# Kernel tuning notes

Hardware: AMD Instinct MI355X
Metric: run time of the kernel (lower is better)

## Reference

```python
import jax, jax.numpy as jnp
import numpy as np

W = 0.5  # loss weight from __init__
EPS = 1e-14


def gradient_l2_loss(x):
    """Mean squared forward finite-difference along each spatial axis of (B,s,r,c)."""
    loss = 0.0
    for ax in (1, 2, 3):
        d = jnp.diff(x, axis=ax)
        loss = loss + jnp.mean(d * d)
    return loss


def setup_inputs() -> dict:
    key = jax.random.key(0)
    k1, k2 = jax.random.split(key)
    B, S, R, C = 2, 128, 128, 128
    L = jax.random.normal(k1, (B, 3, S, R, C), dtype=jnp.float32)
    U = jax.random.normal(k2, (B, 9, S, R, C), dtype=jnp.float32)
    return {"L": L, "U": U}


def reference(L, U):
    B, _, S, R, C = U.shape
    # torch.sort(L, dim=1, descending=True) -> indices[:,0] == argmax over the 3 eigenvalues
    idx0 = jnp.argmax(L, axis=1)  # (B,S,R,C) int
    # U channel layout U{row}_{col}: reshape to (B, col=3, row=3, S,R,C)
    Uview = U.reshape(B, 3, 3, S, R, C)
    idx = jnp.broadcast_to(idx0[:, None, None], (B, 3, 1, S, R, C))
    # faithful to original gather(dim=2)[:, :, 0]
    major = jnp.take_along_axis(Uview, idx, axis=2)[:, :, 0]  # (B,3,S,R,C)
    am = jnp.abs(major)
    den = jnp.sum(am * am, axis=1)  # (B,S,R,C)
    den = jnp.where(den < EPS, EPS, den)
    e1, e2, e3 = am[:, 0], am[:, 1], am[:, 2]
    CO = jnp.sqrt(0.5 * ((e1 - e2) ** 2 + (e2 - e3) ** 2 + (e3 - e1) ** 2) / den)
    CO_grad = 0.0
    for i in range(9):  # fixed small channel loop
        CO_grad = CO_grad + gradient_l2_loss(U[:, i])
    return (CO + CO_grad).mean() * W
```

## Files before the change

kernel.cpp:

```cpp
#include <hip/hip_runtime.h>

#define SS 128
#define RR 128
#define CC 128
#define EPSF 1e-14f

__global__ __launch_bounds__(256) void scol_main(const float* __restrict__ L,
                                                 const float* __restrict__ U,
                                                 float4* __restrict__ part,
                                                 int nvec) {
    const int SRC = SS * RR * CC;
    const int CV = CC / 4;

    float a_co = 0.f, a_ds = 0.f, a_dr = 0.f, a_dc = 0.f;

    int t = blockIdx.x * blockDim.x + threadIdx.x;
    if (t < nvec) {
        int c4 = t % CV;
        int r  = (t / CV) % RR;
        int s  = (t / (CV * RR)) % SS;
        int b  = t / (CV * RR * SS);
        int c  = c4 * 4;

        int pos    = ((s * RR) + r) * CC + c;
        int base_l = b * 3 * SRC + pos;
        int base_u = b * 9 * SRC + pos;

        float4 l0 = *(const float4*)(L + base_l);
        float4 l1 = *(const float4*)(L + base_l + SRC);
        float4 l2 = *(const float4*)(L + base_l + 2 * SRC);
        float L0[4] = {l0.x, l0.y, l0.z, l0.w};
        float L1[4] = {l1.x, l1.y, l1.z, l1.w};
        float L2[4] = {l2.x, l2.y, l2.z, l2.w};
        int idx[4];
#pragma unroll
        for (int j = 0; j < 4; ++j) {
            int id = 0;
            float best = L0[j];
            if (L1[j] > best) { best = L1[j]; id = 1; }
            if (L2[j] > best) { best = L2[j]; id = 2; }
            idx[j] = id;
        }

        float am[3][4];
#pragma unroll
        for (int g = 0; g < 3; ++g)
#pragma unroll
            for (int j = 0; j < 4; ++j) am[g][j] = 0.f;

        bool has_c = (c4 < CV - 1);
        bool has_r = (r < RR - 1);
        bool has_s = (s < SS - 1);

#pragma unroll
        for (int ch = 0; ch < 9; ++ch) {
            int o = base_u + ch * SRC;
            float4 u = *(const float4*)(U + o);
            float uu[4] = {u.x, u.y, u.z, u.w};

            int g = ch / 3, m = ch % 3;
#pragma unroll
            for (int j = 0; j < 4; ++j)
                if (idx[j] == m) am[g][j] = fabsf(uu[j]);

            float d;
            d = u.y - u.x; a_dc += d * d;
            d = u.z - u.y; a_dc += d * d;
            d = u.w - u.z; a_dc += d * d;
            if (has_c) { float un = U[o + 4]; d = un - u.w; a_dc += d * d; }
            if (has_r) {
                float4 ur = *(const float4*)(U + o + CC);
                d = ur.x - u.x; a_dr += d * d;
                d = ur.y - u.y; a_dr += d * d;
                d = ur.z - u.z; a_dr += d * d;
                d = ur.w - u.w; a_dr += d * d;
            }
            if (has_s) {
                float4 us = *(const float4*)(U + o + RR * CC);
                d = us.x - u.x; a_ds += d * d;
                d = us.y - u.y; a_ds += d * d;
                d = us.z - u.z; a_ds += d * d;
                d = us.w - u.w; a_ds += d * d;
            }
        }

#pragma unroll
        for (int j = 0; j < 4; ++j) {
            float e1 = am[0][j], e2 = am[1][j], e3 = am[2][j];
            float den = e1 * e1 + e2 * e2 + e3 * e3;
            den = fmaxf(den, EPSF);
            float num = 0.5f * ((e1 - e2) * (e1 - e2) + (e2 - e3) * (e2 - e3) +
                                (e3 - e1) * (e3 - e1));
            a_co += sqrtf(num / den);
        }
    }

#pragma unroll
    for (int off = 32; off > 0; off >>= 1) {
        a_co += __shfl_down(a_co, off);
        a_ds += __shfl_down(a_ds, off);
        a_dr += __shfl_down(a_dr, off);
        a_dc += __shfl_down(a_dc, off);
    }

    __shared__ float s_co[4], s_ds[4], s_dr[4], s_dc[4];
    int wid = threadIdx.x >> 6;
    int lane = threadIdx.x & 63;
    if (lane == 0) {
        s_co[wid] = a_co; s_ds[wid] = a_ds;
        s_dr[wid] = a_dr; s_dc[wid] = a_dc;
    }
    __syncthreads();
    if (threadIdx.x == 0) {
        float t_co = 0.f, t_ds = 0.f, t_dr = 0.f, t_dc = 0.f;
        for (int w = 0; w < 4; ++w) {
            t_co += s_co[w]; t_ds += s_ds[w];
            t_dr += s_dr[w]; t_dc += s_dc[w];
        }
        part[blockIdx.x] = make_float4(t_co, t_ds, t_dr, t_dc);
    }
}

__global__ __launch_bounds__(256) void scol_final(const float4* __restrict__ part,
                                                  float* __restrict__ out,
                                                  int nblk, int B) {
    double d_co = 0., d_ds = 0., d_dr = 0., d_dc = 0.;
    for (int i = threadIdx.x; i < nblk; i += blockDim.x) {
        float4 p = part[i];
        d_co += (double)p.x; d_ds += (double)p.y;
        d_dr += (double)p.z; d_dc += (double)p.w;
    }
#pragma unroll
    for (int off = 32; off > 0; off >>= 1) {
        d_co += __shfl_down(d_co, off);
        d_ds += __shfl_down(d_ds, off);
        d_dr += __shfl_down(d_dr, off);
        d_dc += __shfl_down(d_dc, off);
    }
    __shared__ double sh[4][4];
    int wid = threadIdx.x >> 6;
    int lane = threadIdx.x & 63;
    if (lane == 0) {
        sh[wid][0] = d_co; sh[wid][1] = d_ds;
        sh[wid][2] = d_dr; sh[wid][3] = d_dc;
    }
    __syncthreads();
    if (threadIdx.x == 0) {
        double t_co = 0., t_ds = 0., t_dr = 0., t_dc = 0.;
        for (int w = 0; w < 4; ++w) {
            t_co += sh[w][0]; t_ds += sh[w][1];
            t_dr += sh[w][2]; t_dc += sh[w][3];
        }
        double nvox = (double)B * SS * RR * CC;
        double nds  = (double)B * (SS - 1) * RR * CC;
        double ndr  = (double)B * SS * (RR - 1) * CC;
        double ndc  = (double)B * SS * RR * (CC - 1);
        out[0] = (float)(0.5 * (t_co / nvox + t_ds / nds + t_dr / ndr + t_dc / ndc));
    }
}

extern "C" void kernel_launch(void* const* d_in, const int* in_sizes, int n_in,
                              void* d_out, int out_size, void* d_ws, size_t ws_size,
                              hipStream_t stream) {
    const float* L = (const float*)d_in[0];
    const float* U = (const float*)d_in[1];
    float* out = (float*)d_out;

    int B = in_sizes[1] / (9 * SS * RR * CC);
    int nvec = B * SS * RR * (CC / 4);

    int threads = 256;
    int blocks = (nvec + threads - 1) / threads;

    float4* part = (float4*)d_ws;

    hipLaunchKernelGGL(scol_main, dim3(blocks), dim3(threads), 0, stream,
                       L, U, part, nvec);
    hipLaunchKernelGGL(scol_final, dim3(1), dim3(threads), 0, stream,
                       part, out, blocks, B);
}
```

Measured before the change: 252.8 us.

## Hoist all U loads up front, use lane shuffle for column neighbor, branchless edges

Restructures the main kernel so each thread issues all 9 center, row-neighbor and slice-neighbor float4 loads before any arithmetic, raising memory-level parallelism. The scalar column-neighbor load is replaced by a wavefront shuffle from the adjacent lane. Edge conditions become clamped offsets and 0/1 weights, so there are no branches. This costs more registers (27 float4 held live), which the launch bounds of 2 are meant to cap.

Result: faster. 245.4 us (-3.0%).

```diff
diff --git a/kernel.cpp b/kernel.cpp
--- a/kernel.cpp
+++ b/kernel.cpp
@@ -5,94 +5,110 @@
 #define CC 128
 #define EPSF 1e-14f
 
-__global__ __launch_bounds__(256) void scol_main(const float* __restrict__ L,
-                                                 const float* __restrict__ U,
-                                                 float4* __restrict__ part,
-                                                 int nvec) {
+__global__ __launch_bounds__(256, 2) void scol_main(const float* __restrict__ L,
+                                                    const float* __restrict__ U,
+                                                    float4* __restrict__ part) {
     const int SRC = SS * RR * CC;
-    const int CV = CC / 4;
 
-    float a_co = 0.f, a_ds = 0.f, a_dr = 0.f, a_dc = 0.f;
+    int tid = threadIdx.x;
+    int c4  = tid & 31;
+    int row = blockIdx.x * 8 + (tid >> 5);
+    int r   = row & (RR - 1);
+    int sr  = row >> 7;
+    int s   = sr & (SS - 1);
+    int b   = sr >> 7;
+    int c   = c4 << 2;
 
-    int t = blockIdx.x * blockDim.x + threadIdx.x;
-    if (t < nvec) {
-        int c4 = t % CV;
-        int r  = (t / CV) % RR;
-        int s  = (t / (CV * RR)) % SS;
-        int b  = t / (CV * RR * SS);
-        int c  = c4 * 4;
+    int pos    = (row - b * (SS * RR)) * CC + c;
+    int base_l = b * 3 * SRC + pos;
+    int base_u = b * 9 * SRC + pos;
 
-        int pos    = ((s * RR) + r) * CC + c;
-        int base_l = b * 3 * SRC + pos;
-        int base_u = b * 9 * SRC + pos;
+    bool  hr = (r < RR - 1), hs = (s < SS - 1), hc = (c4 < 31);
+    float wr = hr ? 1.f : 0.f;
+    float ws = hs ? 1.f : 0.f;
+    float wc = hc ? 1.f : 0.f;
+    int offr = hr ? CC : 0;
+    int offs = hs ? RR * CC : 0;
 
-        float4 l0 = *(const float4*)(L + base_l);
-        float4 l1 = *(const float4*)(L + base_l + SRC);
-        float4 l2 = *(const float4*)(L + base_l + 2 * SRC);
-        float L0[4] = {l0.x, l0.y, l0.z, l0.w};
-        float L1[4] = {l1.x, l1.y, l1.z, l1.w};
-        float L2[4] = {l2.x, l2.y, l2.z, l2.w};
-        int idx[4];
+    float4 l0 = *(const float4*)(L + base_l);
+    float4 l1 = *(const float4*)(L + base_l + SRC);
+    float4 l2 = *(const float4*)(L + base_l + 2 * SRC);
+
+    float4 u[9], ur[9], us[9];
 #pragma unroll
-        for (int j = 0; j < 4; ++j) {
-            int id = 0;
-            float best = L0[j];
-            if (L1[j] > best) { best = L1[j]; id = 1; }
-            if (L2[j] > best) { best = L2[j]; id = 2; }
-            idx[j] = id;
-        }
+    for (int ch = 0; ch < 9; ++ch) {
+        const float* p = U + base_u + ch * SRC;
+        u[ch] = *(const float4*)(p);
+    }
+#pragma unroll
+    for (int ch = 0; ch < 9; ++ch) {
+        const float* p = U + base_u + ch * SRC;
+        ur[ch] = *(const float4*)(p + offr);
+        us[ch] = *(const float4*)(p + offs);
+    }
 
-        float am[3][4];
+    float L0[4] = {l0.x, l0.y, l0.z, l0.w};
+    float L1[4] = {l1.x, l1.y, l1.z, l1.w};
+    float L2[4] = {l2.x, l2.y, l2.z, l2.w};
+    int idx[4];
 #pragma unroll
-        for (int g = 0; g < 3; ++g)
+    for (int j = 0; j < 4; ++j) {
+        int id = 0;
+        float best = L0[j];
+        if (L1[j] > best) { best = L1[j]; id = 1; }
+        if (L2[j] > best) { best = L2[j]; id = 2; }
+        idx[j] = id;
+    }
+
+    float am[3][4];
 #pragma unroll
-            for (int j = 0; j < 4; ++j) am[g][j] = 0.f;
+    for (int g = 0; g < 3; ++g)
+#pragma unroll
+        for (int j = 0; j < 4; ++j) am[g][j] = 0.f;
 
-        bool has_c = (c4 < CV - 1);
-        bool has_r = (r < RR - 1);
-        bool has_s = (s < SS - 1);
+    float a_dc = 0.f, t_dcb = 0.f, t_dr = 0.f, t_ds = 0.f;
 
 #pragma unroll
-        for (int ch = 0; ch < 9; ++ch) {
-            int o = base_u + ch * SRC;
-            float4 u = *(const float4*)(U + o);
-            float uu[4] = {u.x, u.y, u.z, u.w};
+    for (int ch = 0; ch < 9; ++ch) {
+        float4 uu = u[ch];
+        float uuv[4] = {uu.x, uu.y, uu.z, uu.w};
+        int g = ch / 3, m = ch % 3;
+#pragma unroll
+        for (int j = 0; j < 4; ++j)
+            if (idx[j] == m) am[g][j] = fabsf(uuv[j]);
 
-            int g = ch / 3, m = ch % 3;
+        float d;
+        d = uu.y - uu.x; a_dc += d * d;
+        d = uu.z - uu.y; a_dc += d * d;
+        d = uu.w - uu.z; a_dc += d * d;
+        float un = __shfl_down(uu.x, 1);
+        d = un - uu.w; t_dcb += d * d;
+
+        float4 R4 = ur[ch];
+        d = R4.x - uu.x; t_dr += d * d;
+        d = R4.y - uu.y; t_dr += d * d;
+        d = R4.z - uu.z; t_dr += d * d;
+        d = R4.w - uu.w; t_dr += d * d;
+
+        float4 S4 = us[ch];
+        d = S4.x - uu.x; t_ds += d * d;
+        d = S4.y - uu.y; t_ds += d * d;
+        d = S4.z - uu.z; t_ds += d * d;
+        d = S4.w - uu.w; t_ds += d * d;
+    }
+    a_dc += wc * t_dcb;
+    float a_dr = wr * t_dr;
+    float a_ds = ws * t_ds;
+
+    float a_co = 0.f;
 #pragma unroll
-            for (int j = 0; j < 4; ++j)
-                if (idx[j] == m) am[g][j] = fabsf(uu[j]);
-
-            float d;
-            d = u.y - u.x; a_dc += d * d;
-            d = u.z - u.y; a_dc += d * d;
-            d = u.w - u.z; a_dc += d * d;
-            if (has_c) { float un = U[o + 4]; d = un - u.w; a_dc += d * d; }
-            if (has_r) {
-                float4 ur = *(const float4*)(U + o + CC);
-                d = ur.x - u.x; a_dr += d * d;
-                d = ur.y - u.y; a_dr += d * d;
-                d = ur.z - u.z; a_dr += d * d;
-                d = ur.w - u.w; a_dr += d * d;
-            }
-            if (has_s) {
-                float4 us = *(const float4*)(U + o + RR * CC);
-                d = us.x - u.x; a_ds += d * d;
-                d = us.y - u.y; a_ds += d * d;
-                d = us.z - u.z; a_ds += d * d;
-                d = us.w - u.w; a_ds += d * d;
-            }
-        }
-
-#pragma unroll
-        for (int j = 0; j < 4; ++j) {
-            float e1 = am[0][j], e2 = am[1][j], e3 = am[2][j];
-            float den = e1 * e1 + e2 * e2 + e3 * e3;
-            den = fmaxf(den, EPSF);
-            float num = 0.5f * ((e1 - e2) * (e1 - e2) + (e2 - e3) * (e2 - e3) +
-                                (e3 - e1) * (e3 - e1));
-            a_co += sqrtf(num / den);
-        }
+    for (int j = 0; j < 4; ++j) {
+        float e1 = am[0][j], e2 = am[1][j], e3 = am[2][j];
+        float den = e1 * e1 + e2 * e2 + e3 * e3;
+        den = fmaxf(den, EPSF);
+        float num = 0.5f * ((e1 - e2) * (e1 - e2) + (e2 - e3) * (e2 - e3) +
+                            (e3 - e1) * (e3 - e1));
+        a_co += sqrtf(num / den);
     }
 
 #pragma unroll
@@ -104,7 +120,7 @@
     }
 
     __shared__ float s_co[4], s_ds[4], s_dr[4], s_dc[4];
-    int wid = threadIdx.x >> 6;
+    int wid  = threadIdx.x >> 6;
     int lane = threadIdx.x & 63;
     if (lane == 0) {
         s_co[wid] = a_co; s_ds[wid] = a_ds;
@@ -112,12 +128,12 @@
     }
     __syncthreads();
     if (threadIdx.x == 0) {
-        float t_co = 0.f, t_ds = 0.f, t_dr = 0.f, t_dc = 0.f;
+        float t_co = 0.f, t_s = 0.f, t_r = 0.f, t_c = 0.f;
         for (int w = 0; w < 4; ++w) {
-            t_co += s_co[w]; t_ds += s_ds[w];
-            t_dr += s_dr[w]; t_dc += s_dc[w];
+            t_co += s_co[w]; t_s += s_ds[w];
+            t_r += s_dr[w]; t_c += s_dc[w];
         }
-        part[blockIdx.x] = make_float4(t_co, t_ds, t_dr, t_dc);
+        part[blockIdx.x] = make_float4(t_co, t_s, t_r, t_c);
     }
 }
 
@@ -138,7 +154,7 @@
         d_dc += __shfl_down(d_dc, off);
     }
     __shared__ double sh[4][4];
-    int wid = threadIdx.x >> 6;
+    int wid  = threadIdx.x >> 6;
     int lane = threadIdx.x & 63;
     if (lane == 0) {
         sh[wid][0] = d_co; sh[wid][1] = d_ds;
@@ -167,15 +183,13 @@
     float* out = (float*)d_out;
 
     int B = in_sizes[1] / (9 * SS * RR * CC);
-    int nvec = B * SS * RR * (CC / 4);
-
-    int threads = 256;
-    int blocks = (nvec + threads - 1) / threads;
+    int nrow = B * SS * RR;
+    int blocks = nrow / 8;
 
     float4* part = (float4*)d_ws;
 
-    hipLaunchKernelGGL(scol_main, dim3(blocks), dim3(threads), 0, stream,
-                       L, U, part, nvec);
-    hipLaunchKernelGGL(scol_final, dim3(1), dim3(threads), 0, stream,
+    hipLaunchKernelGGL(scol_main, dim3(blocks), dim3(256), 0, stream,
+                       L, U, part);
+    hipLaunchKernelGGL(scol_final, dim3(1), dim3(256), 0, stream,
                        part, out, blocks, B);
 }
```

## Stream s-slabs through double-buffered LDS with async global-to-LDS loads

Applied to the files above, without the earlier changes.

Replaces the one-thread-per-voxel-vector kernel with blocks that each own a 4-row by 8-slice tile. The tile is streamed along s with double-buffered LDS filled by global_load_lds DMA, and the previous slice is kept in registers for the s-difference. This removes the redundant neighbour reads in r and s, which roughly tripled U traffic, and overlaps the next slice's load with compute. The cost is fewer blocks (1024 of 128 threads), which lowers parallelism, plus per-slice barriers. It also depends on exact LDS layout indexing for the boundary row.

Result: slower. 261.8 us (+3.6%).

```diff
diff --git a/kernel.cpp b/kernel.cpp
--- a/kernel.cpp
+++ b/kernel.cpp
@@ -1,92 +1,149 @@
 #include <hip/hip_runtime.h>
+#include <stdint.h>
 
 #define SS 128
 #define RR 128
 #define CC 128
+#define RC (RR * CC)
+#define SRC (SS * RC)
+#define LS 8
 #define EPSF 1e-14f
 
-__global__ __launch_bounds__(256) void scol_main(const float* __restrict__ L,
-                                                 const float* __restrict__ U,
-                                                 float4* __restrict__ part,
-                                                 int nvec) {
-    const int SRC = SS * RR * CC;
-    const int CV = CC / 4;
+#define SLAB_F 4608
+#define BND_F 1152
+#define BUF_F (SLAB_F + BND_F)
+
+__device__ __forceinline__ void dma16(const float* g, float* l) {
+    __builtin_amdgcn_global_load_lds(
+        (const __attribute__((address_space(1))) uint32_t*)g,
+        (__attribute__((address_space(3))) uint32_t*)l,
+        16, 0, 0);
+}
+
+__global__ __launch_bounds__(128, 4) void scol_main(const float* __restrict__ L,
+                                                    const float* __restrict__ U,
+                                                    float4* __restrict__ part) {
+    __shared__ float lds[2][BUF_F];
+    __shared__ float sred[2][4];
+
+    const int tid = threadIdx.x;
+    const int c4  = tid & 31;
+    const int row = tid >> 5;
+
+    int g   = blockIdx.x;
+    int rcI = g & 31;
+    int scI = (g >> 5) & 15;
+    int b   = g >> 9;
+
+    int r0 = rcI << 2;
+    int s0 = scI << 3;
+    int r  = r0 + row;
+    int c  = c4 << 2;
+
+    const float* Ub = U + (size_t)b * 9 * SRC;
+    const float* Lb = L + (size_t)b * 3 * SRC;
+
+    float wc = (c4 < 31) ? 1.f : 0.f;
+    float wr = (r < RR - 1) ? 1.f : 0.f;
+    int rowb = (r0 + 4 < RR) ? (r0 + 4) : (RR - 1);
+
+    float4 uprev[9];
+    {
+        int sprev = (s0 > 0) ? (s0 - 1) : 0;
+        const float* p = Ub + sprev * RC + r * CC + c;
+#pragma unroll
+        for (int ch = 0; ch < 9; ++ch)
+            uprev[ch] = *(const float4*)(p + ch * SRC);
+    }
+
+    {
+        float* dst = &lds[0][0];
+        const float* srcP = Ub + s0 * RC + r0 * CC;
+#pragma unroll
+        for (int ch = 0; ch < 9; ++ch)
+            dma16(srcP + ch * SRC + tid * 4, dst + ch * 512 + tid * 4);
+        const float* srcB = Ub + s0 * RC + rowb * CC;
+        int chp = tid >> 5, col = c4 << 2;
+        dma16(srcB + chp * SRC + col,       dst + SLAB_F + tid * 4);
+        dma16(srcB + (chp + 4) * SRC + col, dst + SLAB_F + 512 + tid * 4);
+        if (tid < 32)
+            dma16(srcB + 8 * SRC + col,     dst + SLAB_F + 1024 + tid * 4);
+    }
 
     float a_co = 0.f, a_ds = 0.f, a_dr = 0.f, a_dc = 0.f;
 
-    int t = blockIdx.x * blockDim.x + threadIdx.x;
-    if (t < nvec) {
-        int c4 = t % CV;
-        int r  = (t / CV) % RR;
-        int s  = (t / (CV * RR)) % SS;
-        int b  = t / (CV * RR * SS);
-        int c  = c4 * 4;
-
-        int pos    = ((s * RR) + r) * CC + c;
-        int base_l = b * 3 * SRC + pos;
-        int base_u = b * 9 * SRC + pos;
-
-        float4 l0 = *(const float4*)(L + base_l);
-        float4 l1 = *(const float4*)(L + base_l + SRC);
-        float4 l2 = *(const float4*)(L + base_l + 2 * SRC);
-        float L0[4] = {l0.x, l0.y, l0.z, l0.w};
-        float L1[4] = {l1.x, l1.y, l1.z, l1.w};
-        float L2[4] = {l2.x, l2.y, l2.z, l2.w};
-        int idx[4];
+    for (int i = 0; i < LS; ++i) {
+        int s  = s0 + i;
+        int bb = i & 1;
+
+        __syncthreads();
+
+        if (i < LS - 1) {
+            float* dst = &lds[bb ^ 1][0];
+            int sp = s + 1;
+            const float* srcP = Ub + sp * RC + r0 * CC;
+#pragma unroll
+            for (int ch = 0; ch < 9; ++ch)
+                dma16(srcP + ch * SRC + tid * 4, dst + ch * 512 + tid * 4);
+            const float* srcB = Ub + sp * RC + rowb * CC;
+            int chp = tid >> 5, col = c4 << 2;
+            dma16(srcB + chp * SRC + col,       dst + SLAB_F + tid * 4);
+            dma16(srcB + (chp + 4) * SRC + col, dst + SLAB_F + 512 + tid * 4);
+            if (tid < 32)
+                dma16(srcB + 8 * SRC + col,     dst + SLAB_F + 1024 + tid * 4);
+        }
+
+        const float* lp = Lb + s * RC + r * CC + c;
+        float4 l0 = *(const float4*)(lp);
+        float4 l1 = *(const float4*)(lp + SRC);
+        float4 l2 = *(const float4*)(lp + 2 * SRC);
+
+        const float* buf  = &lds[bb][0];
+        const float* ownB = buf + row * 128 + c;
+        const float* rnB  = (row < 3) ? (buf + (row + 1) * 128 + c)
+                                      : (buf + SLAB_F + c);
+        int rnStride = (row < 3) ? 512 : 128;
+
+        float wsd = (s > 0) ? 1.f : 0.f;
+
+        float t_ds = 0.f, t_dr = 0.f, t_dcb = 0.f;
+#pragma unroll
+        for (int ch = 0; ch < 9; ++ch) {
+            float4 own = *(const float4*)(ownB + ch * 512);
+            float4 rn  = *(const float4*)(rnB + ch * rnStride);
+            float  cn  = *(ownB + ch * 512 + 4);
+            float d;
+            d = own.y - own.x; a_dc += d * d;
+            d = own.z - own.y; a_dc += d * d;
+            d = own.w - own.z; a_dc += d * d;
+            d = cn    - own.w; t_dcb += d * d;
+            d = rn.x - own.x; t_dr += d * d;
+            d = rn.y - own.y; t_dr += d * d;
+            d = rn.z - own.z; t_dr += d * d;
+            d = rn.w - own.w; t_dr += d * d;
+            float4 up = uprev[ch];
+            d = own.x - up.x; t_ds += d * d;
+            d = own.y - up.y; t_ds += d * d;
+            d = own.z - up.z; t_ds += d * d;
+            d = own.w - up.w; t_ds += d * d;
+            uprev[ch] = own;
+        }
+        a_dc += wc * t_dcb;
+        a_dr += wr * t_dr;
+        a_ds += wsd * t_ds;
+
+        float Lv0[4] = {l0.x, l0.y, l0.z, l0.w};
+        float Lv1[4] = {l1.x, l1.y, l1.z, l1.w};
+        float Lv2[4] = {l2.x, l2.y, l2.z, l2.w};
 #pragma unroll
         for (int j = 0; j < 4; ++j) {
             int id = 0;
-            float best = L0[j];
-            if (L1[j] > best) { best = L1[j]; id = 1; }
-            if (L2[j] > best) { best = L2[j]; id = 2; }
-            idx[j] = id;
-        }
-
-        float am[3][4];
-#pragma unroll
-        for (int g = 0; g < 3; ++g)
-#pragma unroll
-            for (int j = 0; j < 4; ++j) am[g][j] = 0.f;
-
-        bool has_c = (c4 < CV - 1);
-        bool has_r = (r < RR - 1);
-        bool has_s = (s < SS - 1);
-
-#pragma unroll
-        for (int ch = 0; ch < 9; ++ch) {
-            int o = base_u + ch * SRC;
-            float4 u = *(const float4*)(U + o);
-            float uu[4] = {u.x, u.y, u.z, u.w};
-
-            int g = ch / 3, m = ch % 3;
-#pragma unroll
-            for (int j = 0; j < 4; ++j)
-                if (idx[j] == m) am[g][j] = fabsf(uu[j]);
-
-            float d;
-            d = u.y - u.x; a_dc += d * d;
-            d = u.z - u.y; a_dc += d * d;
-            d = u.w - u.z; a_dc += d * d;
-            if (has_c) { float un = U[o + 4]; d = un - u.w; a_dc += d * d; }
-            if (has_r) {
-                float4 ur = *(const float4*)(U + o + CC);
-                d = ur.x - u.x; a_dr += d * d;
-                d = ur.y - u.y; a_dr += d * d;
-                d = ur.z - u.z; a_dr += d * d;
-                d = ur.w - u.w; a_dr += d * d;
-            }
-            if (has_s) {
-                float4 us = *(const float4*)(U + o + RR * CC);
-                d = us.x - u.x; a_ds += d * d;
-                d = us.y - u.y; a_ds += d * d;
-                d = us.z - u.z; a_ds += d * d;
-                d = us.w - u.w; a_ds += d * d;
-            }
-        }
-
-#pragma unroll
-        for (int j = 0; j < 4; ++j) {
-            float e1 = am[0][j], e2 = am[1][j], e3 = am[2][j];
+            float best = Lv0[j];
+            if (Lv1[j] > best) { best = Lv1[j]; id = 1; }
+            if (Lv2[j] > best) { best = Lv2[j]; id = 2; }
+            float e1 = fabsf(*(ownB + (0 + id) * 512 + j));
+            float e2 = fabsf(*(ownB + (3 + id) * 512 + j));
+            float e3 = fabsf(*(ownB + (6 + id) * 512 + j));
             float den = e1 * e1 + e2 * e2 + e3 * e3;
             den = fmaxf(den, EPSF);
             float num = 0.5f * ((e1 - e2) * (e1 - e2) + (e2 - e3) * (e2 - e3) +
@@ -102,22 +159,17 @@
         a_dr += __shfl_down(a_dr, off);
         a_dc += __shfl_down(a_dc, off);
     }
-
-    __shared__ float s_co[4], s_ds[4], s_dr[4], s_dc[4];
-    int wid = threadIdx.x >> 6;
-    int lane = threadIdx.x & 63;
+    int wid = tid >> 6, lane = tid & 63;
     if (lane == 0) {
-        s_co[wid] = a_co; s_ds[wid] = a_ds;
-        s_dr[wid] = a_dr; s_dc[wid] = a_dc;
+        sred[wid][0] = a_co; sred[wid][1] = a_ds;
+        sred[wid][2] = a_dr; sred[wid][3] = a_dc;
     }
     __syncthreads();
-    if (threadIdx.x == 0) {
-        float t_co = 0.f, t_ds = 0.f, t_dr = 0.f, t_dc = 0.f;
-        for (int w = 0; w < 4; ++w) {
-            t_co += s_co[w]; t_ds += s_ds[w];
-            t_dr += s_dr[w]; t_dc += s_dc[w];
-        }
-        part[blockIdx.x] = make_float4(t_co, t_ds, t_dr, t_dc);
+    if (tid == 0) {
+        part[blockIdx.x] = make_float4(sred[0][0] + sred[1][0],
+                                       sred[0][1] + sred[1][1],
+                                       sred[0][2] + sred[1][2],
+                                       sred[0][3] + sred[1][3]);
     }
 }
 
@@ -138,8 +190,7 @@
         d_dc += __shfl_down(d_dc, off);
     }
     __shared__ double sh[4][4];
-    int wid = threadIdx.x >> 6;
-    int lane = threadIdx.x & 63;
+    int wid = threadIdx.x >> 6, lane = threadIdx.x & 63;
     if (lane == 0) {
         sh[wid][0] = d_co; sh[wid][1] = d_ds;
         sh[wid][2] = d_dr; sh[wid][3] = d_dc;
@@ -167,15 +218,12 @@
     float* out = (float*)d_out;
 
     int B = in_sizes[1] / (9 * SS * RR * CC);
-    int nvec = B * SS * RR * (CC / 4);
-
-    int threads = 256;
-    int blocks = (nvec + threads - 1) / threads;
+    int blocks = B * 32 * 16;
 
     float4* part = (float4*)d_ws;
 
-    hipLaunchKernelGGL(scol_main, dim3(blocks), dim3(threads), 0, stream,
-                       L, U, part, nvec);
-    hipLaunchKernelGGL(scol_final, dim3(1), dim3(threads), 0, stream,
+    hipLaunchKernelGGL(scol_main, dim3(blocks), dim3(128), 0, stream,
+                       L, U, part);
+    hipLaunchKernelGGL(scol_final, dim3(1), dim3(256), 0, stream,
                        part, out, blocks, B);
 }
```

## Split work across wavefronts by channel group with LDS exchange for argmax gather

Applied to the files above, without the earlier changes.

Each block now covers two rows of one slice. Three wavefronts each load one group of three U channels and compute its finite differences, while the fourth wavefront loads L and computes the argmax indices. Results are exchanged through shared memory and the CO term is computed by the L wave. The column-edge neighbour now comes from a wave shuffle instead of a scalar reload, branches are replaced by multiplicative masks, block ids are remapped XCD-aware, and the final reduction uses 1024 threads. This aims to raise memory-level parallelism and cut redundant loads, at the cost of two extra block barriers and uneven load across the four waves.

Result: no change. 249.8 us (-1.2%).

```diff
diff --git a/kernel.cpp b/kernel.cpp
--- a/kernel.cpp
+++ b/kernel.cpp
@@ -3,94 +3,136 @@
 #define SS 128
 #define RR 128
 #define CC 128
+#define RC (RR * CC)
+#define VOL (SS * RC)
 #define EPSF 1e-14f
 
-__global__ __launch_bounds__(256) void scol_main(const float* __restrict__ L,
-                                                 const float* __restrict__ U,
-                                                 float4* __restrict__ part,
-                                                 int nvec) {
-    const int SRC = SS * RR * CC;
-    const int CV = CC / 4;
+__global__ __launch_bounds__(256, 8) void scol_main(const float* __restrict__ L,
+                                                    const float* __restrict__ U,
+                                                    float4* __restrict__ part,
+                                                    int nblocks) {
+    __shared__ int    lidx[64];
+    __shared__ float4 lde[3][64];
+    __shared__ float  sred[4][4];
+
+    const int tid  = threadIdx.x;
+    const int wid  = tid >> 6;
+    const int lane = tid & 63;
+    const int half = lane >> 5;
+    const int c4   = lane & 31;
+
+    int id = blockIdx.x;
+    if ((nblocks & 7) == 0) {
+        int per = nblocks >> 3;
+        id = (blockIdx.x & 7) * per + (blockIdx.x >> 3);
+    }
+
+    int rp = id & 63;
+    int s  = (id >> 6) & (SS - 1);
+    int b  = id / (64 * SS);
+
+    int r = rp * 2 + half;
+    int c = c4 << 2;
+
+    float wc = (c4 < 31) ? 1.f : 0.f;
+    float wr = (r < RR - 1) ? 1.f : 0.f;
+    float ws = (s < SS - 1) ? 1.f : 0.f;
+    int offr = (r < RR - 1) ? CC : 0;
+    int offs = (s < SS - 1) ? RC : 0;
+
+    size_t posPlane = (size_t)s * RC + (size_t)r * CC + c;
 
     float a_co = 0.f, a_ds = 0.f, a_dr = 0.f, a_dc = 0.f;
 
-    int t = blockIdx.x * blockDim.x + threadIdx.x;
-    if (t < nvec) {
-        int c4 = t % CV;
-        int r  = (t / CV) % RR;
-        int s  = (t / (CV * RR)) % SS;
-        int b  = t / (CV * RR * SS);
-        int c  = c4 * 4;
-
-        int pos    = ((s * RR) + r) * CC + c;
-        int base_l = b * 3 * SRC + pos;
-        int base_u = b * 9 * SRC + pos;
-
-        float4 l0 = *(const float4*)(L + base_l);
-        float4 l1 = *(const float4*)(L + base_l + SRC);
-        float4 l2 = *(const float4*)(L + base_l + 2 * SRC);
-        float L0[4] = {l0.x, l0.y, l0.z, l0.w};
-        float L1[4] = {l1.x, l1.y, l1.z, l1.w};
-        float L2[4] = {l2.x, l2.y, l2.z, l2.w};
-        int idx[4];
+    float4 own[3];
+
+    if (wid < 3) {
+        const float* p0 = U + ((size_t)(b * 9 + 3 * wid)) * VOL + posPlane;
+        float4 sn[3], rn[3];
+#pragma unroll
+        for (int k = 0; k < 3; ++k) {
+            const float* p = p0 + (size_t)k * VOL;
+            own[k] = *(const float4*)(p);
+            sn[k]  = *(const float4*)(p + offs);
+            rn[k]  = *(const float4*)(p + offr);
+        }
+        float t_dcb = 0.f, t_dr = 0.f, t_ds = 0.f;
+#pragma unroll
+        for (int k = 0; k < 3; ++k) {
+            float4 o = own[k];
+            float d;
+            d = o.y - o.x; a_dc += d * d;
+            d = o.z - o.y; a_dc += d * d;
+            d = o.w - o.z; a_dc += d * d;
+            float cn = __shfl_down(o.x, 1);
+            d = cn - o.w; t_dcb += d * d;
+            float4 R4 = rn[k];
+            d = R4.x - o.x; t_dr += d * d;
+            d = R4.y - o.y; t_dr += d * d;
+            d = R4.z - o.z; t_dr += d * d;
+            d = R4.w - o.w; t_dr += d * d;
+            float4 S4 = sn[k];
+            d = S4.x - o.x; t_ds += d * d;
+            d = S4.y - o.y; t_ds += d * d;
+            d = S4.z - o.z; t_ds += d * d;
+            d = S4.w - o.w; t_ds += d * d;
+        }
+        a_dc += wc * t_dcb;
+        a_dr  = wr * t_dr;
+        a_ds  = ws * t_ds;
+    } else {
+        const float* lp = L + ((size_t)(b * 3)) * VOL + posPlane;
+        float4 l0 = *(const float4*)(lp);
+        float4 l1 = *(const float4*)(lp + VOL);
+        float4 l2 = *(const float4*)(lp + 2 * VOL);
+        float A0[4] = {l0.x, l0.y, l0.z, l0.w};
+        float A1[4] = {l1.x, l1.y, l1.z, l1.w};
+        float A2[4] = {l2.x, l2.y, l2.z, l2.w};
+        int pk = 0;
 #pragma unroll
         for (int j = 0; j < 4; ++j) {
-            int id = 0;
-            float best = L0[j];
-            if (L1[j] > best) { best = L1[j]; id = 1; }
-            if (L2[j] > best) { best = L2[j]; id = 2; }
-            idx[j] = id;
-        }
-
-        float am[3][4];
-#pragma unroll
-        for (int g = 0; g < 3; ++g)
-#pragma unroll
-            for (int j = 0; j < 4; ++j) am[g][j] = 0.f;
-
-        bool has_c = (c4 < CV - 1);
-        bool has_r = (r < RR - 1);
-        bool has_s = (s < SS - 1);
-
-#pragma unroll
-        for (int ch = 0; ch < 9; ++ch) {
-            int o = base_u + ch * SRC;
-            float4 u = *(const float4*)(U + o);
-            float uu[4] = {u.x, u.y, u.z, u.w};
-
-            int g = ch / 3, m = ch % 3;
-#pragma unroll
-            for (int j = 0; j < 4; ++j)
-                if (idx[j] == m) am[g][j] = fabsf(uu[j]);
-
-            float d;
-            d = u.y - u.x; a_dc += d * d;
-            d = u.z - u.y; a_dc += d * d;
-            d = u.w - u.z; a_dc += d * d;
-            if (has_c) { float un = U[o + 4]; d = un - u.w; a_dc += d * d; }
-            if (has_r) {
-                float4 ur = *(const float4*)(U + o + CC);
-                d = ur.x - u.x; a_dr += d * d;
-                d = ur.y - u.y; a_dr += d * d;
-                d = ur.z - u.z; a_dr += d * d;
-                d = ur.w - u.w; a_dr += d * d;
-            }
-            if (has_s) {
-                float4 us = *(const float4*)(U + o + RR * CC);
-                d = us.x - u.x; a_ds += d * d;
-                d = us.y - u.y; a_ds += d * d;
-                d = us.z - u.z; a_ds += d * d;
-                d = us.w - u.w; a_ds += d * d;
-            }
-        }
-
+            int idj = 0;
+            float best = A0[j];
+            if (A1[j] > best) { best = A1[j]; idj = 1; }
+            if (A2[j] > best) { idj = 2; }
+            pk |= idj << (2 * j);
+        }
+        lidx[lane] = pk;
+    }
+
+    __syncthreads();
+
+    if (wid < 3) {
+        int pk = lidx[lane];
+        float e[4];
+        float O0[4] = {own[0].x, own[0].y, own[0].z, own[0].w};
+        float O1[4] = {own[1].x, own[1].y, own[1].z, own[1].w};
+        float O2[4] = {own[2].x, own[2].y, own[2].z, own[2].w};
 #pragma unroll
         for (int j = 0; j < 4; ++j) {
-            float e1 = am[0][j], e2 = am[1][j], e3 = am[2][j];
-            float den = e1 * e1 + e2 * e2 + e3 * e3;
+            int m = (pk >> (2 * j)) & 3;
+            float v = (m == 0) ? O0[j] : (m == 1) ? O1[j] : O2[j];
+            e[j] = fabsf(v);
+        }
+        lde[wid][lane] = make_float4(e[0], e[1], e[2], e[3]);
+    }
+
+    __syncthreads();
+
+    if (wid == 3) {
+        float4 e0 = lde[0][lane];
+        float4 e1 = lde[1][lane];
+        float4 e2 = lde[2][lane];
+        float E0[4] = {e0.x, e0.y, e0.z, e0.w};
+        float E1[4] = {e1.x, e1.y, e1.z, e1.w};
+        float E2[4] = {e2.x, e2.y, e2.z, e2.w};
+#pragma unroll
+        for (int j = 0; j < 4; ++j) {
+            float x = E0[j], y = E1[j], z = E2[j];
+            float den = x * x + y * y + z * z;
             den = fmaxf(den, EPSF);
-            float num = 0.5f * ((e1 - e2) * (e1 - e2) + (e2 - e3) * (e2 - e3) +
-                                (e3 - e1) * (e3 - e1));
+            float num = 0.5f * ((x - y) * (x - y) + (y - z) * (y - z) +
+                                (z - x) * (z - x));
             a_co += sqrtf(num / den);
         }
     }
@@ -102,28 +144,25 @@
         a_dr += __shfl_down(a_dr, off);
         a_dc += __shfl_down(a_dc, off);
     }
-
-    __shared__ float s_co[4], s_ds[4], s_dr[4], s_dc[4];
-    int wid = threadIdx.x >> 6;
-    int lane = threadIdx.x & 63;
     if (lane == 0) {
-        s_co[wid] = a_co; s_ds[wid] = a_ds;
-        s_dr[wid] = a_dr; s_dc[wid] = a_dc;
-    }
-    __syncthreads();
-    if (threadIdx.x == 0) {
-        float t_co = 0.f, t_ds = 0.f, t_dr = 0.f, t_dc = 0.f;
+        sred[wid][0] = a_co; sred[wid][1] = a_ds;
+        sred[wid][2] = a_dr; sred[wid][3] = a_dc;
+    }
+    __syncthreads();
+    if (tid == 0) {
+        float t_co = 0.f, t_s = 0.f, t_r = 0.f, t_c = 0.f;
+#pragma unroll
         for (int w = 0; w < 4; ++w) {
-            t_co += s_co[w]; t_ds += s_ds[w];
-            t_dr += s_dr[w]; t_dc += s_dc[w];
-        }
-        part[blockIdx.x] = make_float4(t_co, t_ds, t_dr, t_dc);
+            t_co += sred[w][0]; t_s += sred[w][1];
+            t_r += sred[w][2]; t_c += sred[w][3];
+        }
+        part[blockIdx.x] = make_float4(t_co, t_s, t_r, t_c);
     }
 }
 
-__global__ __launch_bounds__(256) void scol_final(const float4* __restrict__ part,
-                                                  float* __restrict__ out,
-                                                  int nblk, int B) {
+__global__ __launch_bounds__(1024) void scol_final(const float4* __restrict__ part,
+                                                   float* __restrict__ out,
+                                                   int nblk, int B) {
     double d_co = 0., d_ds = 0., d_dr = 0., d_dc = 0.;
     for (int i = threadIdx.x; i < nblk; i += blockDim.x) {
         float4 p = part[i];
@@ -137,9 +176,8 @@
         d_dr += __shfl_down(d_dr, off);
         d_dc += __shfl_down(d_dc, off);
     }
-    __shared__ double sh[4][4];
-    int wid = threadIdx.x >> 6;
-    int lane = threadIdx.x & 63;
+    __shared__ double sh[16][4];
+    int wid = threadIdx.x >> 6, lane = threadIdx.x & 63;
     if (lane == 0) {
         sh[wid][0] = d_co; sh[wid][1] = d_ds;
         sh[wid][2] = d_dr; sh[wid][3] = d_dc;
@@ -147,7 +185,8 @@
     __syncthreads();
     if (threadIdx.x == 0) {
         double t_co = 0., t_ds = 0., t_dr = 0., t_dc = 0.;
-        for (int w = 0; w < 4; ++w) {
+        int nw = blockDim.x >> 6;
+        for (int w = 0; w < nw; ++w) {
             t_co += sh[w][0]; t_ds += sh[w][1];
             t_dr += sh[w][2]; t_dc += sh[w][3];
         }
@@ -167,15 +206,12 @@
     float* out = (float*)d_out;
 
     int B = in_sizes[1] / (9 * SS * RR * CC);
-    int nvec = B * SS * RR * (CC / 4);
-
-    int threads = 256;
-    int blocks = (nvec + threads - 1) / threads;
+    int nblocks = B * SS * (RR / 2);
 
     float4* part = (float4*)d_ws;
 
-    hipLaunchKernelGGL(scol_main, dim3(blocks), dim3(threads), 0, stream,
-                       L, U, part, nvec);
-    hipLaunchKernelGGL(scol_final, dim3(1), dim3(threads), 0, stream,
-                       part, out, blocks, B);
+    hipLaunchKernelGGL(scol_main, dim3(nblocks), dim3(256), 0, stream,
+                       L, U, part, nblocks);
+    hipLaunchKernelGGL(scol_final, dim3(1), dim3(1024), 0, stream,
+                       part, out, nblocks, B);
 }
```
